# Kernel tuning notes

Hardware: AMD Instinct MI355X
Metric: run time of the kernel (lower is better)

Reference implementation:

```python
import jax, jax.numpy as jnp
import numpy as np

IN_F, OUT_F = 128, 128
B, N = 4, 4096

def setup_inputs() -> dict:
    key = jax.random.key(0)
    k1, k2, k3 = jax.random.split(key, 3)
    relation_matrix = jax.random.uniform(k1, (B, N, N), dtype=jnp.float32)
    inputs = jax.random.normal(k2, (B, N, IN_F), dtype=jnp.float32)
    w = jax.random.normal(k3, (IN_F, OUT_F), dtype=jnp.float32)
    return {"relation_matrix": relation_matrix, "inputs": inputs, "w": w}

def reference(relation_matrix, inputs, w):
    # deg_i = sum_j A_ij ; D = diag(deg) + I  -> inverse is elementwise reciprocal
    deg = jnp.sum(relation_matrix, axis=-1) + 1.0            # [B, N]
    # (A + I) @ X  == A @ X + X  (avoids materializing A + eye)
    ax = jnp.einsum('bnm,bmf->bnf', relation_matrix, inputs) + inputs  # [B, N, in]
    z = (ax / deg[..., None]) @ w                            # [B, N, out]
    return jax.nn.relu(z)
```

## Files before the change

### kernel.cpp

```cpp
#include <hip/hip_runtime.h>
#include <hip/hip_bf16.h>
#include <stdint.h>

#define NN 4096
#define NF 128
#define NB 4
#define KC 256
#define NSTAGE (NN / KC)

typedef __attribute__((ext_vector_type(4))) float  floatx4;
typedef __attribute__((ext_vector_type(8))) __bf16 bf16x8;

__device__ __forceinline__ void load_lds_16(const float* g, float* l) {
    __builtin_amdgcn_global_load_lds(
        (const __attribute__((address_space(1))) uint32_t*)g,
        (__attribute__((address_space(3))) uint32_t*)l, 16, 0, 0);
}

__global__ __launch_bounds__(256) void prep_kernel(const float* __restrict__ X,
                                                   const float* __restrict__ w,
                                                   __bf16* __restrict__ Xpack,
                                                   __bf16* __restrict__ wpack) {
    __shared__ float Xs[32][129];
    const int tid = threadIdx.x;
    const int bx  = blockIdx.x;
    if (bx == 512) {
        for (int p = tid; p < 512; p += 256) {
            int kc = p >> 7, n = p & 127;
#pragma unroll
            for (int k8 = 0; k8 < 32; k8 += 8) {
                bf16x8 v;
#pragma unroll
                for (int j = 0; j < 8; j++)
                    v[j] = (__bf16)w[(size_t)(kc * 32 + k8 + j) * NF + n];
                *(bf16x8*)(wpack + ((size_t)(kc * 128 + n)) * 32 + k8) = v;
            }
        }
        return;
    }
    const int b  = bx >> 7;
    const int kc = bx & 127;
    const float* Xt = X + ((size_t)b * NN + (size_t)kc * 32) * NF;
#pragma unroll
    for (int j = 0; j < 16; j++) {
        int i = tid + j * 256;
        Xs[i >> 7][i & 127] = Xt[i];
    }
    __syncthreads();
    const int f  = tid >> 1;
    const int kh = (tid & 1) * 16;
    bf16x8 v0, v1;
#pragma unroll
    for (int j = 0; j < 8; j++) v0[j] = (__bf16)Xs[kh + j][f];
#pragma unroll
    for (int j = 0; j < 8; j++) v1[j] = (__bf16)Xs[kh + 8 + j][f];
    __bf16* op = Xpack + (((size_t)b * 128 + kc) * 128 + f) * 32 + kh;
    *(bf16x8*)op = v0;
    *(bf16x8*)(op + 8) = v1;
}

__global__ __launch_bounds__(256, 4) void main_kernel(const float* __restrict__ A,
                                                      const float* __restrict__ X,
                                                      const __bf16* __restrict__ Xpack,
                                                      const __bf16* __restrict__ wpack,
                                                      float* __restrict__ out) {
    __shared__ float  At[2][16][260];
    __shared__ __bf16 Us[16][136];

    const int tid  = threadIdx.x;
    const int wv   = tid >> 6;
    const int lane = tid & 63;
    const int lm   = lane & 15;
    const int quad = lane >> 4;

    const int b  = blockIdx.x >> 8;
    const int m0 = (blockIdx.x & 255) << 4;

    const float* Ag[4];
#pragma unroll
    for (int j = 0; j < 4; j++)
        Ag[j] = A + ((size_t)b * NN + m0 + wv * 4 + j) * NN + lane * 4;

    const __bf16* Bbase = Xpack + ((size_t)b * 128 * NF + (wv * 32 + lm)) * 32 + quad * 8;

    floatx4 acc0 = {0.f, 0.f, 0.f, 0.f};
    floatx4 acc1 = {0.f, 0.f, 0.f, 0.f};
    float dsum = 0.f;

#pragma unroll
    for (int j = 0; j < 4; j++)
        load_lds_16(Ag[j], &At[0][wv * 4 + j][0]);

    for (int s = 0; s < NSTAGE; s++) {
        const int buf = s & 1;
        __builtin_amdgcn_s_waitcnt(0x0f70);
        __syncthreads();
        if (s + 1 < NSTAGE) {
#pragma unroll
            for (int j = 0; j < 4; j++)
                load_lds_16(Ag[j] + (size_t)(s + 1) * KC, &At[buf ^ 1][wv * 4 + j][0]);
        }
        const __bf16* Bs = Bbase + (size_t)s * 8 * 4096;
#pragma unroll
        for (int kk = 0; kk < 8; kk++) {
            bf16x8 b0 = *(const bf16x8*)(Bs + (size_t)kk * 4096);
            bf16x8 b1 = *(const bf16x8*)(Bs + (size_t)kk * 4096 + 512);
            floatx4 a0 = *(const floatx4*)&At[buf][lm][kk * 32 + quad * 8];
            floatx4 a1 = *(const floatx4*)&At[buf][lm][kk * 32 + quad * 8 + 4];
            dsum += a0[0] + a0[1] + a0[2] + a0[3] + a1[0] + a1[1] + a1[2] + a1[3];
            bf16x8 af;
#pragma unroll
            for (int i = 0; i < 4; i++) af[i] = (__bf16)a0[i];
#pragma unroll
            for (int i = 0; i < 4; i++) af[4 + i] = (__bf16)a1[i];
            acc0 = __builtin_amdgcn_mfma_f32_16x16x32_bf16(af, b0, acc0, 0, 0, 0);
            acc1 = __builtin_amdgcn_mfma_f32_16x16x32_bf16(af, b1, acc1, 0, 0, 0);
        }
    }

    dsum += __shfl_xor(dsum, 16, 64);
    dsum += __shfl_xor(dsum, 32, 64);
    float degv[4];
#pragma unroll
    for (int i = 0; i < 4; i++)
        degv[i] = __shfl(dsum, quad * 4 + i, 64) + 1.0f;

    bf16x8 wf[4][2];
#pragma unroll
    for (int kc2 = 0; kc2 < 4; kc2++)
#pragma unroll
        for (int nt = 0; nt < 2; nt++)
            wf[kc2][nt] = *(const bf16x8*)(wpack +
                ((size_t)(kc2 * 128 + wv * 32 + nt * 16 + lm)) * 32 + quad * 8);

    const float* Xb = X + ((size_t)b * NN + m0) * NF;
#pragma unroll
    for (int nt = 0; nt < 2; nt++) {
        int col = wv * 32 + nt * 16 + lm;
        floatx4 accv = nt ? acc1 : acc0;
#pragma unroll
        for (int i = 0; i < 4; i++) {
            int r = quad * 4 + i;
            float u = (accv[i] + Xb[(size_t)r * NF + col]) / degv[i];
            Us[r][col] = (__bf16)u;
        }
    }
    __syncthreads();

    floatx4 z0 = {0.f, 0.f, 0.f, 0.f};
    floatx4 z1 = {0.f, 0.f, 0.f, 0.f};
#pragma unroll
    for (int kc2 = 0; kc2 < 4; kc2++) {
        bf16x8 ua = *(const bf16x8*)&Us[lm][kc2 * 32 + quad * 8];
        z0 = __builtin_amdgcn_mfma_f32_16x16x32_bf16(ua, wf[kc2][0], z0, 0, 0, 0);
        z1 = __builtin_amdgcn_mfma_f32_16x16x32_bf16(ua, wf[kc2][1], z1, 0, 0, 0);
    }

    float* ob = out + ((size_t)b * NN + m0) * NF;
#pragma unroll
    for (int nt = 0; nt < 2; nt++) {
        int col = wv * 32 + nt * 16 + lm;
        floatx4 zv = nt ? z1 : z0;
#pragma unroll
        for (int i = 0; i < 4; i++) {
            int r = quad * 4 + i;
            float v = zv[i];
            ob[(size_t)r * NF + col] = v > 0.f ? v : 0.f;
        }
    }
}

extern "C" void kernel_launch(void* const* d_in, const int* in_sizes, int n_in,
                              void* d_out, int out_size, void* d_ws, size_t ws_size,
                              hipStream_t stream) {
    const float* A = (const float*)d_in[0];
    const float* X = (const float*)d_in[1];
    const float* w = (const float*)d_in[2];
    float* out = (float*)d_out;

    __bf16* Xpack = (__bf16*)d_ws;
    __bf16* wpack = Xpack + (size_t)NB * NF * NN;

    prep_kernel<<<513, 256, 0, stream>>>(X, w, Xpack, wpack);
    main_kernel<<<1024, 256, 0, stream>>>(A, X, Xpack, wpack, out);
}
```

Measured before the change: 399.2 us.

## Enlarge block row tile to 64 rows with 8 waves to cut X reloads

```diff
diff --git a/kernel.cpp b/kernel.cpp
--- a/kernel.cpp
+++ b/kernel.cpp
@@ -5,7 +5,7 @@
 #define NN 4096
 #define NF 128
 #define NB 4
-#define KC 256
+#define KC 128
 #define NSTAGE (NN / KC)
 
 typedef __attribute__((ext_vector_type(4))) float  floatx4;
@@ -59,37 +59,44 @@
     *(bf16x8*)(op + 8) = v1;
 }
 
-__global__ __launch_bounds__(256, 4) void main_kernel(const float* __restrict__ A,
+__global__ __launch_bounds__(512, 2) void main_kernel(const float* __restrict__ A,
                                                       const float* __restrict__ X,
                                                       const __bf16* __restrict__ Xpack,
                                                       const __bf16* __restrict__ wpack,
                                                       float* __restrict__ out) {
-    __shared__ float  At[2][16][260];
-    __shared__ __bf16 Us[16][136];
+    __shared__ float  At[2][32][260];
+    __shared__ __bf16 Us[64][136];
 
     const int tid  = threadIdx.x;
     const int wv   = tid >> 6;
     const int lane = tid & 63;
     const int lm   = lane & 15;
     const int quad = lane >> 4;
-
-    const int b  = blockIdx.x >> 8;
-    const int m0 = (blockIdx.x & 255) << 4;
-
-    const float* Ag[4];
+    const int rg   = wv & 1;
+    const int cg   = wv >> 1;
+
+    const int b  = blockIdx.x >> 6;
+    const int m0 = (blockIdx.x & 63) << 6;
+
+    const float* Asrc = A + ((size_t)b * NN + m0 + (lane >> 5)) * NN + (lane & 31) * 4;
+
+    const __bf16* Bbase = Xpack + ((size_t)b * 128 * NF + (cg * 32 + lm)) * 32 + quad * 8;
+
+    floatx4 acc[2][2];
+#pragma unroll
+    for (int i = 0; i < 2; i++)
+#pragma unroll
+        for (int j = 0; j < 2; j++) acc[i][j] = (floatx4){0.f, 0.f, 0.f, 0.f};
+    float ds0 = 0.f, ds1 = 0.f;
+
 #pragma unroll
     for (int j = 0; j < 4; j++)
-        Ag[j] = A + ((size_t)b * NN + m0 + wv * 4 + j) * NN + lane * 4;
-
-    const __bf16* Bbase = Xpack + ((size_t)b * 128 * NF + (wv * 32 + lm)) * 32 + quad * 8;
-
-    floatx4 acc0 = {0.f, 0.f, 0.f, 0.f};
-    floatx4 acc1 = {0.f, 0.f, 0.f, 0.f};
-    float dsum = 0.f;
-
-#pragma unroll
-    for (int j = 0; j < 4; j++)
-        load_lds_16(Ag[j], &At[0][wv * 4 + j][0]);
+        load_lds_16(Asrc + (size_t)(wv * 4 + j) * 2 * NN, &At[0][wv * 4 + j][0]);
+
+    const int r0 = rg * 32 + lm;
+    const int r1 = r0 + 16;
+    const int ofs0 = (r0 & 1) * 128 + quad * 8;
+    const int ofs1 = (r1 & 1) * 128 + quad * 8;
 
     for (int s = 0; s < NSTAGE; s++) {
         const int buf = s & 1;
@@ -98,32 +105,41 @@
         if (s + 1 < NSTAGE) {
 #pragma unroll
             for (int j = 0; j < 4; j++)
-                load_lds_16(Ag[j] + (size_t)(s + 1) * KC, &At[buf ^ 1][wv * 4 + j][0]);
-        }
-        const __bf16* Bs = Bbase + (size_t)s * 8 * 4096;
-#pragma unroll
-        for (int kk = 0; kk < 8; kk++) {
+                load_lds_16(Asrc + (size_t)(wv * 4 + j) * 2 * NN + (size_t)(s + 1) * KC,
+                            &At[buf ^ 1][wv * 4 + j][0]);
+        }
+        const float(*Ab)[260] = At[buf];
+        const __bf16* Bs = Bbase + (size_t)s * 4 * 4096;
+#pragma unroll
+        for (int kk = 0; kk < 4; kk++) {
             bf16x8 b0 = *(const bf16x8*)(Bs + (size_t)kk * 4096);
             bf16x8 b1 = *(const bf16x8*)(Bs + (size_t)kk * 4096 + 512);
-            floatx4 a0 = *(const floatx4*)&At[buf][lm][kk * 32 + quad * 8];
-            floatx4 a1 = *(const floatx4*)&At[buf][lm][kk * 32 + quad * 8 + 4];
-            dsum += a0[0] + a0[1] + a0[2] + a0[3] + a1[0] + a1[1] + a1[2] + a1[3];
-            bf16x8 af;
-#pragma unroll
-            for (int i = 0; i < 4; i++) af[i] = (__bf16)a0[i];
-#pragma unroll
-            for (int i = 0; i < 4; i++) af[4 + i] = (__bf16)a1[i];
-            acc0 = __builtin_amdgcn_mfma_f32_16x16x32_bf16(af, b0, acc0, 0, 0, 0);
-            acc1 = __builtin_amdgcn_mfma_f32_16x16x32_bf16(af, b1, acc1, 0, 0, 0);
-        }
-    }
-
-    dsum += __shfl_xor(dsum, 16, 64);
-    dsum += __shfl_xor(dsum, 32, 64);
-    float degv[4];
-#pragma unroll
-    for (int i = 0; i < 4; i++)
-        degv[i] = __shfl(dsum, quad * 4 + i, 64) + 1.0f;
+            floatx4 a00 = *(const floatx4*)&Ab[r0 >> 1][ofs0 + kk * 32];
+            floatx4 a01 = *(const floatx4*)&Ab[r0 >> 1][ofs0 + kk * 32 + 4];
+            floatx4 a10 = *(const floatx4*)&Ab[r1 >> 1][ofs1 + kk * 32];
+            floatx4 a11 = *(const floatx4*)&Ab[r1 >> 1][ofs1 + kk * 32 + 4];
+            ds0 += a00[0] + a00[1] + a00[2] + a00[3] + a01[0] + a01[1] + a01[2] + a01[3];
+            ds1 += a10[0] + a10[1] + a10[2] + a10[3] + a11[0] + a11[1] + a11[2] + a11[3];
+            bf16x8 af0, af1;
+#pragma unroll
+            for (int i = 0; i < 4; i++) { af0[i] = (__bf16)a00[i]; af0[4 + i] = (__bf16)a01[i]; }
+#pragma unroll
+            for (int i = 0; i < 4; i++) { af1[i] = (__bf16)a10[i]; af1[4 + i] = (__bf16)a11[i]; }
+            acc[0][0] = __builtin_amdgcn_mfma_f32_16x16x32_bf16(af0, b0, acc[0][0], 0, 0, 0);
+            acc[0][1] = __builtin_amdgcn_mfma_f32_16x16x32_bf16(af0, b1, acc[0][1], 0, 0, 0);
+            acc[1][0] = __builtin_amdgcn_mfma_f32_16x16x32_bf16(af1, b0, acc[1][0], 0, 0, 0);
+            acc[1][1] = __builtin_amdgcn_mfma_f32_16x16x32_bf16(af1, b1, acc[1][1], 0, 0, 0);
+        }
+    }
+
+    ds0 += __shfl_xor(ds0, 16, 64); ds0 += __shfl_xor(ds0, 32, 64);
+    ds1 += __shfl_xor(ds1, 16, 64); ds1 += __shfl_xor(ds1, 32, 64);
+    float deg0[4], deg1[4];
+#pragma unroll
+    for (int i = 0; i < 4; i++) {
+        deg0[i] = __shfl(ds0, quad * 4 + i, 64) + 1.0f;
+        deg1[i] = __shfl(ds1, quad * 4 + i, 64) + 1.0f;
+    }
 
     bf16x8 wf[4][2];
 #pragma unroll
@@ -131,41 +147,47 @@
 #pragma unroll
         for (int nt = 0; nt < 2; nt++)
             wf[kc2][nt] = *(const bf16x8*)(wpack +
-                ((size_t)(kc2 * 128 + wv * 32 + nt * 16 + lm)) * 32 + quad * 8);
+                ((size_t)(kc2 * 128 + cg * 32 + nt * 16 + lm)) * 32 + quad * 8);
 
     const float* Xb = X + ((size_t)b * NN + m0) * NF;
 #pragma unroll
-    for (int nt = 0; nt < 2; nt++) {
-        int col = wv * 32 + nt * 16 + lm;
-        floatx4 accv = nt ? acc1 : acc0;
-#pragma unroll
-        for (int i = 0; i < 4; i++) {
-            int r = quad * 4 + i;
-            float u = (accv[i] + Xb[(size_t)r * NF + col]) / degv[i];
-            Us[r][col] = (__bf16)u;
+    for (int sub = 0; sub < 2; sub++) {
+#pragma unroll
+        for (int nt = 0; nt < 2; nt++) {
+            int col = cg * 32 + nt * 16 + lm;
+#pragma unroll
+            for (int i = 0; i < 4; i++) {
+                int r = rg * 32 + sub * 16 + quad * 4 + i;
+                float d = sub ? deg1[i] : deg0[i];
+                float u = (acc[sub][nt][i] + Xb[(size_t)r * NF + col]) / d;
+                Us[r][col] = (__bf16)u;
+            }
         }
     }
     __syncthreads();
 
-    floatx4 z0 = {0.f, 0.f, 0.f, 0.f};
-    floatx4 z1 = {0.f, 0.f, 0.f, 0.f};
-#pragma unroll
-    for (int kc2 = 0; kc2 < 4; kc2++) {
-        bf16x8 ua = *(const bf16x8*)&Us[lm][kc2 * 32 + quad * 8];
-        z0 = __builtin_amdgcn_mfma_f32_16x16x32_bf16(ua, wf[kc2][0], z0, 0, 0, 0);
-        z1 = __builtin_amdgcn_mfma_f32_16x16x32_bf16(ua, wf[kc2][1], z1, 0, 0, 0);
-    }
-
     float* ob = out + ((size_t)b * NN + m0) * NF;
 #pragma unroll
-    for (int nt = 0; nt < 2; nt++) {
-        int col = wv * 32 + nt * 16 + lm;
-        floatx4 zv = nt ? z1 : z0;
-#pragma unroll
-        for (int i = 0; i < 4; i++) {
-            int r = quad * 4 + i;
-            float v = zv[i];
-            ob[(size_t)r * NF + col] = v > 0.f ? v : 0.f;
+    for (int sub = 0; sub < 2; sub++) {
+        int rm = rg * 32 + sub * 16;
+        floatx4 z0 = {0.f, 0.f, 0.f, 0.f};
+        floatx4 z1 = {0.f, 0.f, 0.f, 0.f};
+#pragma unroll
+        for (int kc2 = 0; kc2 < 4; kc2++) {
+            bf16x8 ua = *(const bf16x8*)&Us[rm + lm][kc2 * 32 + quad * 8];
+            z0 = __builtin_amdgcn_mfma_f32_16x16x32_bf16(ua, wf[kc2][0], z0, 0, 0, 0);
+            z1 = __builtin_amdgcn_mfma_f32_16x16x32_bf16(ua, wf[kc2][1], z1, 0, 0, 0);
+        }
+#pragma unroll
+        for (int nt = 0; nt < 2; nt++) {
+            int col = cg * 32 + nt * 16 + lm;
+            floatx4 zv = nt ? z1 : z0;
+#pragma unroll
+            for (int i = 0; i < 4; i++) {
+                int r = rm + quad * 4 + i;
+                float v = zv[i];
+                ob[(size_t)r * NF + col] = v > 0.f ? v : 0.f;
+            }
         }
     }
 }
@@ -182,5 +204,5 @@
     __bf16* wpack = Xpack + (size_t)NB * NF * NN;
 
     prep_kernel<<<513, 256, 0, stream>>>(X, w, Xpack, wpack);
-    main_kernel<<<1024, 256, 0, stream>>>(A, X, Xpack, wpack, out);
-}
+    main_kernel<<<256, 512, 0, stream>>>(A, X, Xpack, wpack, out);
+}
```

Result: faster. 390.1 us (-2.3%).
